# Kernel tuning notes

Hardware: AMD Instinct MI355X
Metric: run time of the kernel (lower is better)

The kernel has to match this reference:

```python
import jax, jax.numpy as jnp
import numpy as np

B, Hg, Wg, DIM, HEADS, WS, SHIFT = 16, 64, 64, 512, 16, 8, 4
HIDDEN = 4 * DIM
PRIOR_BETA = 1.0
EPS = 1e-5


def _layernorm(x, g, b):
    m = jnp.mean(x, axis=-1, keepdims=True)
    v = jnp.mean(jnp.square(x - m), axis=-1, keepdims=True)
    return (x - m) / jnp.sqrt(v + EPS) * g + b


def _rel_pos_index(ws):
    coords = np.stack(np.meshgrid(np.arange(ws), np.arange(ws), indexing='ij')).reshape(2, -1)
    rel = (coords[:, :, None] - coords[:, None, :]).transpose(1, 2, 0)
    rel[..., 0] += ws - 1
    rel[..., 1] += ws - 1
    rel[..., 0] *= 2 * ws - 1
    return rel.sum(-1)  # (N, N) int


def _shift_mask(H, W, ws, shift):
    img = np.zeros((H, W))
    cnt = 0
    for hs in (slice(0, -ws), slice(-ws, -shift), slice(-shift, None)):
        for wsl in (slice(0, -ws), slice(-ws, -shift), slice(-shift, None)):
            img[hs, wsl] = cnt
            cnt += 1
    N = ws * ws
    mw = img.reshape(H // ws, ws, W // ws, ws).transpose(0, 2, 1, 3).reshape(-1, N)
    am = mw[:, None, :] - mw[:, :, None]
    return np.where(am != 0, -100.0, 0.0).astype(np.float32)  # (nW, N, N)


def setup_inputs() -> dict:
    key = jax.random.key(0)
    ks = jax.random.split(key, 8)
    s = 0.02
    return {
        'x': jax.random.normal(ks[0], (B, Hg * Wg, DIM), jnp.float32),
        'M_map': jax.random.uniform(ks[1], (B, Hg, Wg, 1), jnp.float32),
        'norm1_g': jnp.ones((DIM,), jnp.float32),
        'norm1_b': jnp.zeros((DIM,), jnp.float32),
        'qkv_w': jax.random.normal(ks[2], (3 * DIM, DIM), jnp.float32) * s,
        'qkv_b': jnp.zeros((3 * DIM,), jnp.float32),
        'proj_w': jax.random.normal(ks[3], (DIM, DIM), jnp.float32) * s,
        'proj_b': jnp.zeros((DIM,), jnp.float32),
        'rpb_table': jax.random.normal(ks[4], ((2 * WS - 1) ** 2, HEADS), jnp.float32) * s,
        'norm2_g': jnp.ones((DIM,), jnp.float32),
        'norm2_b': jnp.zeros((DIM,), jnp.float32),
        'fc1_w': jax.random.normal(ks[5], (HIDDEN, DIM), jnp.float32) * s,
        'fc1_b': jnp.zeros((HIDDEN,), jnp.float32),
        'fc2_w': jax.random.normal(ks[6], (DIM, HIDDEN), jnp.float32) * s,
        'fc2_b': jnp.zeros((DIM,), jnp.float32),
        'H': Hg,
        'W': Wg,
    }


def reference(x, M_map, norm1_g, norm1_b, qkv_w, qkv_b, proj_w, proj_b, rpb_table,
              norm2_g, norm2_b, fc1_w, fc1_b, fc2_w, fc2_b, H, W):
    Bsz, L, C = x.shape
    ws, shift, heads = WS, SHIFT, HEADS
    N = ws * ws
    hd = C // heads
    scale = hd ** -0.5

    shortcut = x
    y = _layernorm(x, norm1_g, norm1_b).reshape(Bsz, H, W, C)
    Mm = jnp.clip(M_map[..., 0], 0.0, 1.0)  # (B, H, W)

    # cyclic shift (SW-MSA)
    y = jnp.roll(y, (-shift, -shift), axis=(1, 2))
    Mm = jnp.roll(Mm, (-shift, -shift), axis=(1, 2))

    # window partition -> (B*nW, N, C) and (B*nW, N)
    def win_part(t):
        c = t.shape[-1]
        t = t.reshape(Bsz, H // ws, ws, W // ws, ws, c)
        return t.transpose(0, 1, 3, 2, 4, 5).reshape(-1, N, c)

    xw = win_part(y)
    mw = win_part(Mm[..., None])[..., 0]
    B_ = xw.shape[0]

    qkv = (xw @ qkv_w.T + qkv_b).reshape(B_, N, 3, heads, hd).transpose(2, 0, 3, 1, 4)
    q, k, v = qkv[0], qkv[1], qkv[2]  # each (B_, heads, N, hd)
    attn = jnp.einsum('bhnd,bhmd->bhnm', q * scale, k)

    # relative position bias (heads, N, N)
    rpi = _rel_pos_index(ws)
    rpb = rpb_table[rpi.reshape(-1)].reshape(N, N, heads).transpose(2, 0, 1)
    attn = attn + rpb[None]

    # semantic prior bias: 0.5*(M_i + M_j), broadcast over heads
    sb = 0.5 * (mw[:, :, None] + mw[:, None, :])  # (B_, N, N)
    attn = attn + PRIOR_BETA * sb[:, None]

    # shift mask
    am = jnp.asarray(_shift_mask(H, W, ws, shift), attn.dtype)  # (nW, N, N)
    nW = am.shape[0]
    attn = attn.reshape(Bsz, nW, heads, N, N) + am[None, :, None]
    attn = attn.reshape(B_, heads, N, N)

    attn = jax.nn.softmax(attn, axis=-1)
    out = jnp.einsum('bhnm,bhmd->bhnd', attn, v).transpose(0, 2, 1, 3).reshape(B_, N, C)
    out = out @ proj_w.T + proj_b

    # window reverse + reverse shift
    out = out.reshape(Bsz, H // ws, W // ws, ws, ws, C).transpose(0, 1, 3, 2, 4, 5).reshape(Bsz, H, W, C)
    out = jnp.roll(out, (shift, shift), axis=(1, 2)).reshape(Bsz, L, C)

    x1 = shortcut + out
    h = jax.nn.gelu(_layernorm(x1, norm2_g, norm2_b) @ fc1_w.T + fc1_b, approximate=False)
    return x1 + (h @ fc2_w.T + fc2_b)
```

## Files before the change

kernel.cpp:

```cpp
#include <hip/hip_runtime.h>
#include <hip/hip_bf16.h>

typedef unsigned short u16;
typedef unsigned int u32;
typedef __attribute__((ext_vector_type(4))) float f32x4;
typedef __attribute__((ext_vector_type(8))) short bf16x8;

#define DEV static __device__ __forceinline__

DEV float bf2f(u16 u) { u32 x = ((u32)u) << 16; return __builtin_bit_cast(float, x); }
DEV u16 f2bf(float f) {
  __hip_bfloat16 h = __float2bfloat16(f);
  return __builtin_bit_cast(u16, h);
}

DEV float fast_gelu(float x) {
  const float ax = fabsf(x) * 0.70710678118f;
  const float t = __builtin_amdgcn_rcpf(1.0f + 0.3275911f * ax);
  const float poly =
      t * (0.254829592f +
           t * (-0.284496736f + t * (1.421413741f + t * (-1.453152027f + t * 1.061405429f))));
  const float e = __expf(-ax * ax);
  float er = 1.0f - poly * e;
  er = __builtin_copysignf(er, x);
  return 0.5f * x * (1.0f + er);
}

DEV void gld16(const u16* g, u16* l) {
  __builtin_amdgcn_global_load_lds((const __attribute__((address_space(1))) void*)g,
                                   (__attribute__((address_space(3))) void*)l, 16, 0, 0);
}

__global__ void cvt_bf16(const float* __restrict__ s, u16* __restrict__ d, int n) {
  int i = blockIdx.x * 256 + threadIdx.x;
  if (i < n) d[i] = f2bf(s[i]);
}

__global__ __launch_bounds__(256)
void ln_bf16(const float* __restrict__ src, const float* __restrict__ g,
             const float* __restrict__ b, u16* __restrict__ dst) {
  const int row = blockIdx.x * 4 + (threadIdx.x >> 6);
  const int lane = threadIdx.x & 63;
  const float* p = src + (long)row * 512 + lane * 8;
  float x[8];
  *(float4*)&x[0] = *(const float4*)p;
  *(float4*)&x[4] = *(const float4*)(p + 4);
  float s = 0.f;
#pragma unroll
  for (int e = 0; e < 8; ++e) s += x[e];
#pragma unroll
  for (int off = 32; off; off >>= 1) s += __shfl_xor(s, off, 64);
  const float mean = s * (1.0f / 512.0f);
  float q = 0.f;
#pragma unroll
  for (int e = 0; e < 8; ++e) { float d = x[e] - mean; q += d * d; }
#pragma unroll
  for (int off = 32; off; off >>= 1) q += __shfl_xor(q, off, 64);
  const float rinv = rsqrtf(q * (1.0f / 512.0f) + 1e-5f);
  u16 o[8];
  const int c0 = lane * 8;
#pragma unroll
  for (int e = 0; e < 8; ++e) o[e] = f2bf((x[e] - mean) * rinv * g[c0 + e] + b[c0 + e]);
  *(uint4*)(dst + (long)row * 512 + c0) = *(uint4*)o;
}

enum { EPI_QKV = 0, EPI_PROJ = 1, EPI_GELU = 2, EPI_FC2 = 3 };

constexpr int SLOT = 12288;

template <int EPI>
__global__ __launch_bounds__(512, 4)
void gemm256(const u16* __restrict__ A, const u16* __restrict__ W,
             const float* __restrict__ bias, const float* __restrict__ res,
             void* __restrict__ outv, int M, int N, int K) {
  extern __shared__ u16 sm[];
  (void)M;
  const int t = threadIdx.x;
  const int lane = t & 63;
  const int wave = t >> 6;
  const int wm = wave >> 2;
  const int wn = wave & 3;
  const long m0 = (long)blockIdx.y * 128;
  const long n0 = (long)blockIdx.x * 256;

  const int sr = t >> 2;
  const int sc = ((t & 3) ^ ((sr >> 1) & 3)) * 8;
  const u16* gA0 = A + (m0 + sr) * (long)K + sc;
  const u16* gB0 = W + (n0 + sr) * (long)K + sc;
  const u16* gB1 = gB0 + 128L * K;
  u16* lws = sm + wave * 512;

  const int NT = K >> 5;
  f32x4 acc[4][4] = {};
  const int fr = lane & 15;
  const int kp = ((lane >> 4) ^ ((fr >> 1) & 3)) * 8;

#define STAGE(slot, tile)                      \
  do {                                         \
    const int _k = (tile) * 32;                \
    u16* _b = lws + (slot) * SLOT;             \
    gld16(gA0 + _k, _b);                       \
    gld16(gB0 + _k, _b + 4096);                \
    gld16(gB1 + _k, _b + 8192);                \
  } while (0)

#define COMPUTE(slot)                                                                           \
  do {                                                                                          \
    const u16* Ab = sm + (slot) * SLOT + (wm * 64 + fr) * 32 + kp;                              \
    const u16* Bb = sm + (slot) * SLOT + 4096 + (wn * 64 + fr) * 32 + kp;                       \
    bf16x8 af[4], bfv[4];                                                                       \
    _Pragma("unroll")                                                                           \
    for (int i = 0; i < 4; ++i) af[i] = *(const bf16x8*)(Ab + i * 512);                         \
    _Pragma("unroll")                                                                           \
    for (int j = 0; j < 4; ++j) bfv[j] = *(const bf16x8*)(Bb + j * 512);                        \
    __builtin_amdgcn_s_setprio(1);                                                              \
    _Pragma("unroll")                                                                           \
    for (int i = 0; i < 4; ++i)                                                                 \
      _Pragma("unroll")                                                                         \
      for (int j = 0; j < 4; ++j)                                                               \
        acc[i][j] = __builtin_amdgcn_mfma_f32_16x16x32_bf16(af[i], bfv[j], acc[i][j], 0, 0, 0); \
    __builtin_amdgcn_s_setprio(0);                                                              \
  } while (0)

  STAGE(0, 0);
  STAGE(1, 1);
  asm volatile("s_waitcnt vmcnt(3)" ::: "memory");
  __builtin_amdgcn_s_barrier();
  asm volatile("" ::: "memory");

  int cs = 0, ss = 2;
  int kt = 0;
  for (; kt < NT - 2; ++kt) {
    STAGE(ss, kt + 2);
    COMPUTE(cs);
    asm volatile("s_waitcnt vmcnt(3)" ::: "memory");
    __builtin_amdgcn_s_barrier();
    asm volatile("" ::: "memory");
    cs = cs == 2 ? 0 : cs + 1;
    ss = ss == 2 ? 0 : ss + 1;
  }
  COMPUTE(cs);
  asm volatile("s_waitcnt vmcnt(0)" ::: "memory");
  __builtin_amdgcn_s_barrier();
  asm volatile("" ::: "memory");
  cs = cs == 2 ? 0 : cs + 1;
  COMPUTE(cs);
#undef STAGE
#undef COMPUTE

  const int col = lane & 15;
  const int rq = (lane >> 4) * 4;
  const long ncol = n0 + wn * 64 + col;
  float bv[4];
#pragma unroll
  for (int ni = 0; ni < 4; ++ni) bv[ni] = bias[ncol + ni * 16];
#pragma unroll
  for (int mi = 0; mi < 4; ++mi) {
#pragma unroll
    for (int r = 0; r < 4; ++r) {
      const long m = m0 + wm * 64 + mi * 16 + rq + r;
      const long base = m * (long)N + ncol;
      if constexpr (EPI == EPI_QKV) {
        u16* p = (u16*)outv + base;
#pragma unroll
        for (int ni = 0; ni < 4; ++ni) p[ni * 16] = f2bf(acc[mi][ni][r] + bv[ni]);
      } else if constexpr (EPI == EPI_PROJ) {
        float* p = (float*)outv + base;
        const float* rp = res + base;
#pragma unroll
        for (int ni = 0; ni < 4; ++ni) p[ni * 16] = acc[mi][ni][r] + bv[ni] + rp[ni * 16];
      } else if constexpr (EPI == EPI_GELU) {
        u16* p = (u16*)outv + base;
#pragma unroll
        for (int ni = 0; ni < 4; ++ni) p[ni * 16] = f2bf(fast_gelu(acc[mi][ni][r] + bv[ni]));
      } else {
        float* p = (float*)outv + base;
        const float* rp = res + base;
#pragma unroll
        for (int ni = 0; ni < 4; ++ni) p[ni * 16] = acc[mi][ni][r] + bv[ni] + rp[ni * 16];
      }
    }
  }
}

constexpr int SS_S = 68;
constexpr int VT_S = 72;

__global__ __launch_bounds__(256)
void attn_mfma(const u16* __restrict__ qkv, const float* __restrict__ mmap,
               const float* __restrict__ rpb, u16* __restrict__ outp) {
  __shared__ u16 SSb[4 * 64 * SS_S];
  __shared__ u16 Vtb[4 * 32 * VT_S];
  __shared__ u16 rpb_s[16 * 226];
  __shared__ float mw[64];
  __shared__ int tok[64];
  __shared__ int regi[64];

  const int t = threadIdx.x;
  const int lane = t & 63, wave = t >> 6;
  const int c = lane & 15, q = lane >> 4;
  const int win = blockIdx.x;
  const int b = win >> 6, wh = (win >> 3) & 7, ww = win & 7;

  if (t < 64) {
    const int i = t >> 3, j = t & 7;
    const int hs = wh * 8 + i, wsv = ww * 8 + j;
    const int h = (hs + 4) & 63, w = (wsv + 4) & 63;
    const int tk = b * 4096 + h * 64 + w;
    tok[t] = tk;
    mw[t] = fminf(fmaxf(mmap[tk], 0.f), 1.f);
    regi[t] = (hs < 56 ? 0 : (hs < 60 ? 1 : 2)) * 3 + (wsv < 56 ? 0 : (wsv < 60 ? 1 : 2));
  }
  for (int id = t; id < 3600; id += 256) {
    const int h = id & 15, idx = id >> 4;
    rpb_s[h * 226 + idx] = f2bf(rpb[id]);
  }
  __syncthreads();

  u16* SS = SSb + wave * 64 * SS_S;
  u16* Vt = Vtb + wave * 32 * VT_S;

  int tQ[4];
  float mwn[16], mwm[4];
  int rgn[16], rgm[4];
#pragma unroll
  for (int i = 0; i < 4; ++i) tQ[i] = tok[16 * i + c];
#pragma unroll
  for (int i = 0; i < 4; ++i)
#pragma unroll
    for (int r = 0; r < 4; ++r) {
      const int n = 16 * i + 4 * q + r;
      mwn[i * 4 + r] = mw[n];
      rgn[i * 4 + r] = regi[n];
    }
#pragma unroll
  for (int j = 0; j < 4; ++j) {
    const int m = 16 * j + c;
    mwm[j] = mw[m];
    rgm[j] = regi[m];
  }
  const int imc = c >> 3, jmc = c & 7;
  const int tV = tok[lane];
  const float scale = 0.17677669529663687f;

  for (int hi = 0; hi < 4; ++hi) {
    const int head = wave * 4 + hi;

    bf16x8 qf[4], kf[4];
#pragma unroll
    for (int i = 0; i < 4; ++i) {
      const u16* base = qkv + (long)tQ[i] * 1536 + head * 32 + q * 8;
      qf[i] = *(const bf16x8*)(base);
      kf[i] = *(const bf16x8*)(base + 512);
    }

    {
      const u16* vp = qkv + (long)tV * 1536 + 1024 + head * 32;
      u16 vv[32];
      *(uint4*)&vv[0]  = *(const uint4*)(vp);
      *(uint4*)&vv[8]  = *(const uint4*)(vp + 8);
      *(uint4*)&vv[16] = *(const uint4*)(vp + 16);
      *(uint4*)&vv[24] = *(const uint4*)(vp + 24);
#pragma unroll
      for (int d = 0; d < 32; ++d) Vt[d * VT_S + lane] = vv[d];
    }

    f32x4 acc[4][4] = {};
#pragma unroll
    for (int i = 0; i < 4; ++i)
#pragma unroll
      for (int j = 0; j < 4; ++j)
        acc[i][j] = __builtin_amdgcn_mfma_f32_16x16x32_bf16(qf[i], kf[j], acc[i][j], 0, 0, 0);

    const u16* rb = rpb_s + head * 226;
    float rmx[16], rsum[16];
#pragma unroll
    for (int i = 0; i < 4; ++i)
#pragma unroll
      for (int r = 0; r < 4; ++r) {
        const int n = 16 * i + 4 * q + r;
        const int inr = n >> 3, jnr = n & 7;
        float mx = -1e30f;
#pragma unroll
        for (int j = 0; j < 4; ++j) {
          const int di = inr - 2 * j - imc + 7;
          const int dj = jnr - jmc + 7;
          float s = acc[i][j][r] * scale + bf2f(rb[di * 15 + dj]) +
                    0.5f * (mwn[i * 4 + r] + mwm[j]);
          if (rgn[i * 4 + r] != rgm[j]) s -= 100.f;
          acc[i][j][r] = s;
          mx = fmaxf(mx, s);
        }
        rmx[i * 4 + r] = mx;
      }
#pragma unroll
    for (int ir = 0; ir < 16; ++ir)
#pragma unroll
      for (int msk = 1; msk < 16; msk <<= 1)
        rmx[ir] = fmaxf(rmx[ir], __shfl_xor(rmx[ir], msk, 64));
#pragma unroll
    for (int i = 0; i < 4; ++i)
#pragma unroll
      for (int r = 0; r < 4; ++r) {
        float sm = 0.f;
#pragma unroll
        for (int j = 0; j < 4; ++j) {
          const float e = __expf(acc[i][j][r] - rmx[i * 4 + r]);
          acc[i][j][r] = e;
          sm += e;
        }
        rsum[i * 4 + r] = sm;
      }
#pragma unroll
    for (int ir = 0; ir < 16; ++ir) {
#pragma unroll
      for (int msk = 1; msk < 16; msk <<= 1)
        rsum[ir] += __shfl_xor(rsum[ir], msk, 64);
      rsum[ir] = 1.0f / rsum[ir];
    }

#pragma unroll
    for (int i = 0; i < 4; ++i)
#pragma unroll
      for (int j = 0; j < 4; ++j) {
        ushort4 pk;
        pk.x = f2bf(acc[i][j][0] * rsum[i * 4 + 0]);
        pk.y = f2bf(acc[i][j][1] * rsum[i * 4 + 1]);
        pk.z = f2bf(acc[i][j][2] * rsum[i * 4 + 2]);
        pk.w = f2bf(acc[i][j][3] * rsum[i * 4 + 3]);
        *(ushort4*)&SS[(16 * j + c) * SS_S + 16 * i + 4 * q] = pk;
      }

    __syncthreads();

    bf16x8 av[2][2];
#pragma unroll
    for (int mi = 0; mi < 2; ++mi)
#pragma unroll
      for (int ki = 0; ki < 2; ++ki)
        av[mi][ki] = *(const bf16x8*)&Vt[(16 * mi + c) * VT_S + 32 * ki + 8 * q];

    f32x4 oacc[2][4] = {};
#pragma unroll
    for (int ki = 0; ki < 2; ++ki)
#pragma unroll
      for (int ni = 0; ni < 4; ++ni) {
        union { u16 h[8]; bf16x8 v; } ub;
#pragma unroll
        for (int jj = 0; jj < 8; ++jj)
          ub.h[jj] = SS[(32 * ki + 8 * q + jj) * SS_S + 16 * ni + c];
#pragma unroll
        for (int mi = 0; mi < 2; ++mi)
          oacc[mi][ni] = __builtin_amdgcn_mfma_f32_16x16x32_bf16(av[mi][ki], ub.v, oacc[mi][ni], 0, 0, 0);
      }

#pragma unroll
    for (int ni = 0; ni < 4; ++ni) {
      u16* ob = outp + (long)tQ[ni] * 512 + head * 32;
#pragma unroll
      for (int mi = 0; mi < 2; ++mi) {
        ushort4 pk;
        pk.x = f2bf(oacc[mi][ni][0]);
        pk.y = f2bf(oacc[mi][ni][1]);
        pk.z = f2bf(oacc[mi][ni][2]);
        pk.w = f2bf(oacc[mi][ni][3]);
        *(ushort4*)(ob + 16 * mi + 4 * q) = pk;
      }
    }
    __syncthreads();
  }
}

extern "C" void kernel_launch(void* const* d_in, const int* in_sizes, int n_in,
                              void* d_out, int out_size, void* d_ws, size_t ws_size,
                              hipStream_t stream) {
  (void)in_sizes; (void)n_in; (void)out_size; (void)ws_size;
  const float* x      = (const float*)d_in[0];
  const float* mmap   = (const float*)d_in[1];
  const float* n1g    = (const float*)d_in[2];
  const float* n1b    = (const float*)d_in[3];
  const float* qkv_w  = (const float*)d_in[4];
  const float* qkv_b  = (const float*)d_in[5];
  const float* proj_w = (const float*)d_in[6];
  const float* proj_b = (const float*)d_in[7];
  const float* rpb    = (const float*)d_in[8];
  const float* n2g    = (const float*)d_in[9];
  const float* n2b    = (const float*)d_in[10];
  const float* fc1_w  = (const float*)d_in[11];
  const float* fc1_b  = (const float*)d_in[12];
  const float* fc2_w  = (const float*)d_in[13];
  const float* fc2_b  = (const float*)d_in[14];
  float* out = (float*)d_out;
  char* ws = (char*)d_ws;

  u16*   ybf   = (u16*)(ws);
  u16*   qkvbf = (u16*)(ws + (64L  << 20));
  u16*   attno = (u16*)(ws + (256L << 20));
  float* x1    = (float*)(ws + (320L << 20));
  u16*   hbuf  = qkvbf;
  u16*   wqkv  = (u16*)(ws + (448L << 20));
  u16*   wproj = wqkv + 1536 * 512;
  u16*   wfc1  = wproj + 512 * 512;
  u16*   wfc2  = wfc1 + 2048 * 512;

  static bool smem_init = false;
  if (!smem_init) {
    smem_init = true;
    (void)hipFuncSetAttribute(reinterpret_cast<const void*>(gemm256<EPI_QKV>),
                              hipFuncAttributeMaxDynamicSharedMemorySize, 73728);
    (void)hipFuncSetAttribute(reinterpret_cast<const void*>(gemm256<EPI_PROJ>),
                              hipFuncAttributeMaxDynamicSharedMemorySize, 73728);
    (void)hipFuncSetAttribute(reinterpret_cast<const void*>(gemm256<EPI_GELU>),
                              hipFuncAttributeMaxDynamicSharedMemorySize, 73728);
    (void)hipFuncSetAttribute(reinterpret_cast<const void*>(gemm256<EPI_FC2>),
                              hipFuncAttributeMaxDynamicSharedMemorySize, 73728);
  }

  cvt_bf16<<<1536 * 512 / 256, 256, 0, stream>>>(qkv_w, wqkv, 1536 * 512);
  cvt_bf16<<<512 * 512 / 256, 256, 0, stream>>>(proj_w, wproj, 512 * 512);
  cvt_bf16<<<2048 * 512 / 256, 256, 0, stream>>>(fc1_w, wfc1, 2048 * 512);
  cvt_bf16<<<512 * 2048 / 256, 256, 0, stream>>>(fc2_w, wfc2, 512 * 2048);

  ln_bf16<<<16384, 256, 0, stream>>>(x, n1g, n1b, ybf);
  gemm256<EPI_QKV><<<dim3(6, 512), 512, 73728, stream>>>(ybf, wqkv, qkv_b, nullptr, qkvbf, 65536, 1536, 512);
  attn_mfma<<<1024, 256, 0, stream>>>(qkvbf, mmap, rpb, attno);
  gemm256<EPI_PROJ><<<dim3(2, 512), 512, 73728, stream>>>(attno, wproj, proj_b, x, x1, 65536, 512, 512);
  ln_bf16<<<16384, 256, 0, stream>>>(x1, n2g, n2b, ybf);
  gemm256<EPI_GELU><<<dim3(8, 512), 512, 73728, stream>>>(ybf, wfc1, fc1_b, nullptr, hbuf, 65536, 2048, 512);
  gemm256<EPI_FC2><<<dim3(2, 512), 512, 73728, stream>>>(hbuf, wfc2, fc2_b, x1, out, 65536, 512, 2048);
}
```

Before: 1.047 ms.

## Enlarge GEMM tiles to 256x256 with double-buffered 64-wide K stages

The GEMM kernel is rebuilt to compute a 256x256 output tile per block instead of 128x256, with each wave holding 8x4 MFMA accumulators. K is staged 64 at a time into two 64KB LDS buffers, and loads for the next stage are interleaved with MFMA sub-steps under finer barriers. The aim is higher arithmetic intensity per LDS/global load and better overlap of memory with compute. In exchange it uses 128KB LDS, more registers and lower occupancy (2 blocks per CU bound), and the grid has half as many blocks.

```diff
diff --git a/kernel.cpp b/kernel.cpp
--- a/kernel.cpp
+++ b/kernel.cpp
@@ -66,87 +66,147 @@
 
 enum { EPI_QKV = 0, EPI_PROJ = 1, EPI_GELU = 2, EPI_FC2 = 3 };
 
-constexpr int SLOT = 12288;
+constexpr int BUF = 32768;
 
 template <int EPI>
-__global__ __launch_bounds__(512, 4)
-void gemm256(const u16* __restrict__ A, const u16* __restrict__ W,
-             const float* __restrict__ bias, const float* __restrict__ res,
-             void* __restrict__ outv, int M, int N, int K) {
+__global__ __launch_bounds__(512, 2)
+void gemm8p(const u16* __restrict__ A, const u16* __restrict__ W,
+            const float* __restrict__ bias, const float* __restrict__ res,
+            void* __restrict__ outv, int M, int N, int K) {
   extern __shared__ u16 sm[];
   (void)M;
   const int t = threadIdx.x;
-  const int lane = t & 63;
-  const int wave = t >> 6;
+  const int lane = t & 63, wave = t >> 6;
   const int wm = wave >> 2;
   const int wn = wave & 3;
-  const long m0 = (long)blockIdx.y * 128;
+  const long m0 = (long)blockIdx.y * 256;
   const long n0 = (long)blockIdx.x * 256;
 
   const int sr = t >> 2;
-  const int sc = ((t & 3) ^ ((sr >> 1) & 3)) * 8;
+  const int sc = ((t & 3) ^ ((t >> 3) & 3)) * 8;
   const u16* gA0 = A + (m0 + sr) * (long)K + sc;
+  const u16* gA1 = gA0 + 128L * K;
   const u16* gB0 = W + (n0 + sr) * (long)K + sc;
   const u16* gB1 = gB0 + 128L * K;
-  u16* lws = sm + wave * 512;
-
-  const int NT = K >> 5;
-  f32x4 acc[4][4] = {};
+  u16* smw = sm + wave * 512;
+
+  const int NT = K >> 6;
+  f32x4 acc[8][4] = {};
   const int fr = lane & 15;
-  const int kp = ((lane >> 4) ^ ((fr >> 1) & 3)) * 8;
-
-#define STAGE(slot, tile)                      \
-  do {                                         \
-    const int _k = (tile) * 32;                \
-    u16* _b = lws + (slot) * SLOT;             \
-    gld16(gA0 + _k, _b);                       \
-    gld16(gB0 + _k, _b + 4096);                \
-    gld16(gB1 + _k, _b + 8192);                \
+  const int ap = ((lane >> 4) ^ ((fr >> 1) & 3)) * 8;
+  const int aB = (wm * 128 + fr) * 32 + ap;
+  const int bB = 16384 + (wn * 64 + fr) * 32 + ap;
+
+  bf16x8 af[8], b0, b1;
+
+#define STG(dst, g0, g1, koff)                  \
+  do {                                          \
+    gld16((g0) + (koff), smw + (dst));          \
+    gld16((g1) + (koff), smw + (dst) + 4096);   \
   } while (0)
 
-#define COMPUTE(slot)                                                                           \
+#define RD_A(ksel, bb)                                                          \
+  _Pragma("unroll") for (int i = 0; i < 8; ++i)                                 \
+      af[i] = *(const bf16x8*)(sm + (bb) * BUF + (ksel) * 8192 + aB + i * 512)
+
+#define RD_B(j, ksel, bb) (*(const bf16x8*)(sm + (bb) * BUF + (ksel) * 8192 + bB + (j) * 512))
+
+#define MFMA16(j0)                                                                              \
   do {                                                                                          \
-    const u16* Ab = sm + (slot) * SLOT + (wm * 64 + fr) * 32 + kp;                              \
-    const u16* Bb = sm + (slot) * SLOT + 4096 + (wn * 64 + fr) * 32 + kp;                       \
-    bf16x8 af[4], bfv[4];                                                                       \
-    _Pragma("unroll")                                                                           \
-    for (int i = 0; i < 4; ++i) af[i] = *(const bf16x8*)(Ab + i * 512);                         \
-    _Pragma("unroll")                                                                           \
-    for (int j = 0; j < 4; ++j) bfv[j] = *(const bf16x8*)(Bb + j * 512);                        \
     __builtin_amdgcn_s_setprio(1);                                                              \
-    _Pragma("unroll")                                                                           \
-    for (int i = 0; i < 4; ++i)                                                                 \
-      _Pragma("unroll")                                                                         \
-      for (int j = 0; j < 4; ++j)                                                               \
-        acc[i][j] = __builtin_amdgcn_mfma_f32_16x16x32_bf16(af[i], bfv[j], acc[i][j], 0, 0, 0); \
+    _Pragma("unroll") for (int i = 0; i < 8; ++i) acc[i][j0] =                                  \
+        __builtin_amdgcn_mfma_f32_16x16x32_bf16(af[i], b0, acc[i][j0], 0, 0, 0);                \
+    _Pragma("unroll") for (int i = 0; i < 8; ++i) acc[i][j0 + 1] =                              \
+        __builtin_amdgcn_mfma_f32_16x16x32_bf16(af[i], b1, acc[i][j0 + 1], 0, 0, 0);            \
     __builtin_amdgcn_s_setprio(0);                                                              \
   } while (0)
 
-  STAGE(0, 0);
-  STAGE(1, 1);
-  asm volatile("s_waitcnt vmcnt(3)" ::: "memory");
-  __builtin_amdgcn_s_barrier();
-  asm volatile("" ::: "memory");
-
-  int cs = 0, ss = 2;
+#define LGKM0()                                            \
+  asm volatile("s_waitcnt lgkmcnt(0)" ::: "memory");       \
+  __builtin_amdgcn_sched_barrier(0)
+
+#define VMBAR4()                                           \
+  asm volatile("s_waitcnt vmcnt(4)" ::: "memory");         \
+  __builtin_amdgcn_s_barrier();                            \
+  asm volatile("" ::: "memory")
+
+#define VMBAR0()                                           \
+  asm volatile("s_waitcnt vmcnt(0)" ::: "memory");         \
+  __builtin_amdgcn_s_barrier();                            \
+  asm volatile("" ::: "memory")
+
+  STG(0, gA0, gA1, 0);
+  STG(16384, gB0, gB1, 0);
+  STG(8192, gA0, gA1, 32);
+  STG(24576, gB0, gB1, 32);
+
   int kt = 0;
-  for (; kt < NT - 2; ++kt) {
-    STAGE(ss, kt + 2);
-    COMPUTE(cs);
-    asm volatile("s_waitcnt vmcnt(3)" ::: "memory");
-    __builtin_amdgcn_s_barrier();
-    asm volatile("" ::: "memory");
-    cs = cs == 2 ? 0 : cs + 1;
-    ss = ss == 2 ? 0 : ss + 1;
-  }
-  COMPUTE(cs);
-  asm volatile("s_waitcnt vmcnt(0)" ::: "memory");
-  __builtin_amdgcn_s_barrier();
-  asm volatile("" ::: "memory");
-  cs = cs == 2 ? 0 : cs + 1;
-  COMPUTE(cs);
-#undef STAGE
-#undef COMPUTE
+  for (; kt < NT - 1; ++kt) {
+    const int bb = kt & 1;
+    const int nbase = (bb ^ 1) * BUF;
+    const int kn = (kt + 1) * 64;
+    VMBAR4();
+    RD_A(0, bb);
+    b0 = RD_B(0, 0, bb);
+    b1 = RD_B(1, 0, bb);
+    STG(nbase, gA0, gA1, kn);
+    LGKM0();
+    MFMA16(0);
+    __builtin_amdgcn_s_barrier();
+    b0 = RD_B(2, 0, bb);
+    b1 = RD_B(3, 0, bb);
+    STG(nbase + 16384, gB0, gB1, kn);
+    LGKM0();
+    MFMA16(2);
+    __builtin_amdgcn_s_barrier();
+    VMBAR4();
+    RD_A(1, bb);
+    b0 = RD_B(0, 1, bb);
+    b1 = RD_B(1, 1, bb);
+    STG(nbase + 8192, gA0, gA1, kn + 32);
+    LGKM0();
+    MFMA16(0);
+    __builtin_amdgcn_s_barrier();
+    b0 = RD_B(2, 1, bb);
+    b1 = RD_B(3, 1, bb);
+    STG(nbase + 24576, gB0, gB1, kn + 32);
+    LGKM0();
+    MFMA16(2);
+    __builtin_amdgcn_s_barrier();
+  }
+  {
+    const int bb = kt & 1;
+    VMBAR4();
+    RD_A(0, bb);
+    b0 = RD_B(0, 0, bb);
+    b1 = RD_B(1, 0, bb);
+    LGKM0();
+    MFMA16(0);
+    __builtin_amdgcn_s_barrier();
+    b0 = RD_B(2, 0, bb);
+    b1 = RD_B(3, 0, bb);
+    LGKM0();
+    MFMA16(2);
+    __builtin_amdgcn_s_barrier();
+    VMBAR0();
+    RD_A(1, bb);
+    b0 = RD_B(0, 1, bb);
+    b1 = RD_B(1, 1, bb);
+    LGKM0();
+    MFMA16(0);
+    __builtin_amdgcn_s_barrier();
+    b0 = RD_B(2, 1, bb);
+    b1 = RD_B(3, 1, bb);
+    LGKM0();
+    MFMA16(2);
+  }
+#undef STG
+#undef RD_A
+#undef RD_B
+#undef MFMA16
+#undef LGKM0
+#undef VMBAR4
+#undef VMBAR0
 
   const int col = lane & 15;
   const int rq = (lane >> 4) * 4;
@@ -155,10 +215,10 @@
 #pragma unroll
   for (int ni = 0; ni < 4; ++ni) bv[ni] = bias[ncol + ni * 16];
 #pragma unroll
-  for (int mi = 0; mi < 4; ++mi) {
+  for (int mi = 0; mi < 8; ++mi) {
 #pragma unroll
     for (int r = 0; r < 4; ++r) {
-      const long m = m0 + wm * 64 + mi * 16 + rq + r;
+      const long m = m0 + wm * 128 + mi * 16 + rq + r;
       const long base = m * (long)N + ncol;
       if constexpr (EPI == EPI_QKV) {
         u16* p = (u16*)outv + base;
@@ -406,14 +466,14 @@
   static bool smem_init = false;
   if (!smem_init) {
     smem_init = true;
-    (void)hipFuncSetAttribute(reinterpret_cast<const void*>(gemm256<EPI_QKV>),
-                              hipFuncAttributeMaxDynamicSharedMemorySize, 73728);
-    (void)hipFuncSetAttribute(reinterpret_cast<const void*>(gemm256<EPI_PROJ>),
-                              hipFuncAttributeMaxDynamicSharedMemorySize, 73728);
-    (void)hipFuncSetAttribute(reinterpret_cast<const void*>(gemm256<EPI_GELU>),
-                              hipFuncAttributeMaxDynamicSharedMemorySize, 73728);
-    (void)hipFuncSetAttribute(reinterpret_cast<const void*>(gemm256<EPI_FC2>),
-                              hipFuncAttributeMaxDynamicSharedMemorySize, 73728);
+    (void)hipFuncSetAttribute(reinterpret_cast<const void*>(gemm8p<EPI_QKV>),
+                              hipFuncAttributeMaxDynamicSharedMemorySize, 131072);
+    (void)hipFuncSetAttribute(reinterpret_cast<const void*>(gemm8p<EPI_PROJ>),
+                              hipFuncAttributeMaxDynamicSharedMemorySize, 131072);
+    (void)hipFuncSetAttribute(reinterpret_cast<const void*>(gemm8p<EPI_GELU>),
+                              hipFuncAttributeMaxDynamicSharedMemorySize, 131072);
+    (void)hipFuncSetAttribute(reinterpret_cast<const void*>(gemm8p<EPI_FC2>),
+                              hipFuncAttributeMaxDynamicSharedMemorySize, 131072);
   }
 
   cvt_bf16<<<1536 * 512 / 256, 256, 0, stream>>>(qkv_w, wqkv, 1536 * 512);
@@ -422,10 +482,10 @@
   cvt_bf16<<<512 * 2048 / 256, 256, 0, stream>>>(fc2_w, wfc2, 512 * 2048);
 
   ln_bf16<<<16384, 256, 0, stream>>>(x, n1g, n1b, ybf);
-  gemm256<EPI_QKV><<<dim3(6, 512), 512, 73728, stream>>>(ybf, wqkv, qkv_b, nullptr, qkvbf, 65536, 1536, 512);
+  gemm8p<EPI_QKV><<<dim3(6, 256), 512, 131072, stream>>>(ybf, wqkv, qkv_b, nullptr, qkvbf, 65536, 1536, 512);
   attn_mfma<<<1024, 256, 0, stream>>>(qkvbf, mmap, rpb, attno);
-  gemm256<EPI_PROJ><<<dim3(2, 512), 512, 73728, stream>>>(attno, wproj, proj_b, x, x1, 65536, 512, 512);
+  gemm8p<EPI_PROJ><<<dim3(2, 256), 512, 131072, stream>>>(attno, wproj, proj_b, x, x1, 65536, 512, 512);
   ln_bf16<<<16384, 256, 0, stream>>>(x1, n2g, n2b, ybf);
-  gemm256<EPI_GELU><<<dim3(8, 512), 512, 73728, stream>>>(ybf, wfc1, fc1_b, nullptr, hbuf, 65536, 2048, 512);
-  gemm256<EPI_FC2><<<dim3(2, 512), 512, 73728, stream>>>(hbuf, wfc2, fc2_b, x1, out, 65536, 512, 2048);
-}
+  gemm8p<EPI_GELU><<<dim3(8, 256), 512, 131072, stream>>>(ybf, wfc1, fc1_b, nullptr, hbuf, 65536, 2048, 512);
+  gemm8p<EPI_FC2><<<dim3(2, 256), 512, 131072, stream>>>(hbuf, wfc2, fc2_b, x1, out, 65536, 512, 2048);
+}
```

Measured after the change: 1.048 ms. Within noise of the previous version (+0.0%).
